# Optimization experiments

Measured on AMD Instinct MI355X. Metric: run time of the kernel, lower is better.

Reference implementation:

```python
import jax, jax.numpy as jnp
import numpy as np
import math

B, T, D, H, L, V = 2, 1024, 768, 12, 4, 50257
HD = D // H
ROPE_PCT = 0.5
MAX_WL = 10000.0
EPS = 1e-5


def setup_inputs() -> dict:
    key = jax.random.key(0)
    ks = jax.random.split(key, 8)
    s = 0.02
    return {
        "idx": jax.random.randint(ks[0], (B, T), 0, V, dtype=jnp.int32),
        "wte": jax.random.normal(ks[1], (V, D), jnp.float32) * s,
        "ln1_g": jnp.ones((L, D), jnp.float32),
        "ln1_b": jnp.zeros((L, D), jnp.float32),
        "Wqkv": jax.random.normal(ks[2], (L, D, 3 * D), jnp.float32) * s,
        "bqkv": jnp.zeros((L, 3 * D), jnp.float32),
        "Wo": jax.random.normal(ks[3], (L, D, D), jnp.float32) * s,
        "bo": jnp.zeros((L, D), jnp.float32),
        "ln2_g": jnp.ones((L, D), jnp.float32),
        "ln2_b": jnp.zeros((L, D), jnp.float32),
        "Wfc": jax.random.normal(ks[4], (L, D, 4 * D), jnp.float32) * s,
        "bfc": jnp.zeros((L, 4 * D), jnp.float32),
        "Wp": jax.random.normal(ks[5], (L, 4 * D, D), jnp.float32) * s,
        "bp": jnp.zeros((L, D), jnp.float32),
        "lnf_g": jnp.ones((D,), jnp.float32),
        "lnf_b": jnp.zeros((D,), jnp.float32),
        "Wlm": jax.random.normal(ks[6], (D, V), jnp.float32) * s,
    }


def _ln(x, g, b):
    m = x.mean(-1, keepdims=True)
    v = x.var(-1, keepdims=True)
    return (x - m) / jnp.sqrt(v + EPS) * g + b


def _gelu(x):
    return 0.5 * x * (1.0 + jnp.tanh(math.sqrt(2.0 / math.pi) * (x + 0.044715 * x ** 3)))


def _p_rope(x, positions):
    # x: [B, H, T, HD]; partial RoPE: rotate first ROPE_PCT of angle pairs, leave rest.
    rope_angles = int(ROPE_PCT * HD // 2)
    nope_angles = HD // 2 - rope_angles
    fraction = 2.0 * jnp.arange(0, rope_angles) / HD
    timescale = jnp.power(MAX_WL, fraction)
    timescale = jnp.pad(timescale, (0, nope_angles), constant_values=jnp.inf)
    sinusoid = positions[:, None] / timescale[None, :]  # [T, HD//2]; pos/inf = 0 -> no rotation
    sin, cos = jnp.sin(sinusoid), jnp.cos(sinusoid)
    first, second = jnp.split(x, 2, axis=-1)
    out = jnp.concatenate([first * cos - second * sin, second * cos + first * sin], axis=-1)
    return out.astype(x.dtype)


def reference(idx, wte, ln1_g, ln1_b, Wqkv, bqkv, Wo, bo, ln2_g, ln2_b, Wfc, bfc, Wp, bp, lnf_g, lnf_b, Wlm):
    x = wte[idx]  # [B, T, D]
    positions = jnp.arange(T, dtype=x.dtype)
    causal = jnp.tril(jnp.ones((T, T), dtype=bool))
    scale = jnp.sqrt(jnp.float32(HD)).astype(x.dtype)
    for l in range(L):
        h1 = _ln(x, ln1_g[l], ln1_b[l])
        h2 = _ln(x, ln2_g[l], ln2_b[l])  # note: both LNs read the same x (as in source)
        # attention
        qkv = h1 @ Wqkv[l] + bqkv[l]
        q, k, v = jnp.split(qkv, 3, axis=-1)
        sh = lambda t: t.reshape(B, T, H, HD).transpose(0, 2, 1, 3)
        q, k, v = sh(q), sh(k), sh(v)
        q = _p_rope(q, positions)
        k = _p_rope(k, positions)
        att = jnp.einsum('bhqd,bhkd->bhqk', q, k) / scale
        att = jnp.where(causal, att, jnp.finfo(att.dtype).min)
        att = jax.nn.softmax(att, axis=-1)
        y = jnp.einsum('bhqk,bhkd->bhqd', att, v)
        y = y.transpose(0, 2, 1, 3).reshape(B, T, D)
        x = x + (y @ Wo[l] + bo[l])
        # MLP
        h = _gelu(h2 @ Wfc[l] + bfc[l])
        x = x + (h @ Wp[l] + bp[l])
    x = _ln(x, lnf_g, lnf_b)
    logits = x @ Wlm  # [B, T, V]
    return logits
```

## Files before the change

### kernel.cpp

```cpp
#include <hip/hip_runtime.h>

typedef unsigned short u16;
typedef unsigned int u32;
typedef __attribute__((ext_vector_type(8))) short bf16x8;
typedef __attribute__((ext_vector_type(4))) float f32x4;

#define SEQ 1024
#define DM 768
#define NH 12
#define HD2 64
#define NLAYER 4
#define NVOCAB 50257
#define BT 2048

__device__ __forceinline__ u16 f2bf(float f) {
  union { float f; u32 u; } v; v.f = f;
  u32 r = v.u + 0x7FFFu + ((v.u >> 16) & 1u);
  return (u16)(r >> 16);
}
__device__ __forceinline__ float bf2f(u16 u) {
  union { u32 u; float f; } v; v.u = ((u32)u) << 16;
  return v.f;
}

__device__ __forceinline__ void glds16(const u16* g, u16* l) {
  __builtin_amdgcn_global_load_lds(
      (const __attribute__((address_space(1))) u32*)(const void*)g,
      (__attribute__((address_space(3))) u32*)(void*)l, 16, 0, 0);
}

__global__ void k_embed(const int* __restrict__ idx, const float* __restrict__ wte,
                        float* __restrict__ xf) {
  int r = blockIdx.x;
  int tok = idx[r];
  const float* s = wte + (size_t)tok * DM;
  float* d = xf + (size_t)r * DM;
  for (int c = threadIdx.x; c < DM; c += 256) d[c] = s[c];
}

__global__ void k_cvtT(const float* __restrict__ in, u16* __restrict__ out,
                       int R, int C) {
  __shared__ u16 t[32][34];
  int c0 = blockIdx.x * 32, r0 = blockIdx.y * 32;
  int tx = threadIdx.x & 31, ty = threadIdx.x >> 5;
#pragma unroll
  for (int i = 0; i < 4; ++i) {
    int r = r0 + ty + i * 8, c = c0 + tx;
    float v = (c < C) ? in[(size_t)r * C + c] : 0.f;
    t[ty + i * 8][tx] = f2bf(v);
  }
  __syncthreads();
  int cy = threadIdx.x >> 4;
  int rx = (threadIdx.x & 15) * 2;
#pragma unroll
  for (int i = 0; i < 2; ++i) {
    int c = c0 + cy + i * 16;
    if (c < C) {
      u32 wv = (u32)t[rx][cy + i * 16] | ((u32)t[rx + 1][cy + i * 16] << 16);
      *(u32*)&out[(size_t)c * R + r0 + rx] = wv;
    }
  }
}

__device__ __forceinline__ float bsum(float v, float* red) {
#pragma unroll
  for (int o = 32; o > 0; o >>= 1) v += __shfl_down(v, o);
  if ((threadIdx.x & 63) == 0) red[threadIdx.x >> 6] = v;
  __syncthreads();
  if (threadIdx.x == 0) red[4] = red[0] + red[1] + red[2] + red[3];
  __syncthreads();
  return red[4];
}

__global__ void k_ln(const float* __restrict__ x, const float* __restrict__ g1,
                     const float* __restrict__ b1, const float* __restrict__ g2,
                     const float* __restrict__ b2, u16* __restrict__ o1,
                     u16* __restrict__ o2) {
  __shared__ float red[8];
  int r = blockIdx.x;
  int t = threadIdx.x;
  const float* xr = x + (size_t)r * DM;
  float v0 = xr[t], v1 = xr[t + 256], v2 = xr[t + 512];
  float mean = bsum(v0 + v1 + v2, red) * (1.f / DM);
  float d0 = v0 - mean, d1 = v1 - mean, d2 = v2 - mean;
  float var = bsum(d0 * d0 + d1 * d1 + d2 * d2, red) * (1.f / DM);
  float rstd = rsqrtf(var + 1e-5f);
  u16* p1 = o1 + (size_t)r * DM;
  p1[t]       = f2bf(d0 * rstd * g1[t]       + b1[t]);
  p1[t + 256] = f2bf(d1 * rstd * g1[t + 256] + b1[t + 256]);
  p1[t + 512] = f2bf(d2 * rstd * g1[t + 512] + b1[t + 512]);
  if (o2) {
    u16* p2 = o2 + (size_t)r * DM;
    p2[t]       = f2bf(d0 * rstd * g2[t]       + b2[t]);
    p2[t + 256] = f2bf(d1 * rstd * g2[t + 256] + b2[t + 256]);
    p2[t + 512] = f2bf(d2 * rstd * g2[t + 512] + b2[t + 512]);
  }
}

__global__ void k_rope(const u16* __restrict__ qkvb, u16* __restrict__ qr,
                       u16* __restrict__ kr) {
  int gid = blockIdx.x * 256 + threadIdx.x;
  int j = gid & 31;
  int h = (gid >> 5) % NH;
  int t = (gid / (32 * NH)) & (SEQ - 1);
  int b = gid / (32 * NH * SEQ);
  float c = 1.f, s = 0.f;
  if (j < 16) {
    float inv = powf(10000.f, -(float)j * (1.f / 32.f));
    float ang = (float)t * inv;
    c = cosf(ang);
    s = sinf(ang);
  }
  size_t base = (size_t)(b * SEQ + t) * (3 * DM);
  size_t ob = ((size_t)(b * NH + h) * SEQ + t) * HD2 + j;
  {
    float a0 = bf2f(qkvb[base + h * HD2 + j]);
    float a1 = bf2f(qkvb[base + h * HD2 + j + 32]);
    qr[ob] = f2bf(a0 * c - a1 * s);
    qr[ob + 32] = f2bf(a1 * c + a0 * s);
  }
  {
    float a0 = bf2f(qkvb[base + DM + h * HD2 + j]);
    float a1 = bf2f(qkvb[base + DM + h * HD2 + j + 32]);
    kr[ob] = f2bf(a0 * c - a1 * s);
    kr[ob + 32] = f2bf(a1 * c + a0 * s);
  }
}

__global__ void k_vtrans(const u16* __restrict__ qkvb, u16* __restrict__ vT) {
  __shared__ u16 tile[64][65];
  int t0 = blockIdx.x * 64;
  int bh = blockIdx.y;
  int b = bh / NH, h = bh % NH;
  int rr = threadIdx.x >> 2, seg = threadIdx.x & 3;
  const u16* src = qkvb + (size_t)(b * SEQ + t0 + rr) * (3 * DM) + 2 * DM + h * HD2;
#pragma unroll
  for (int i = 0; i < 16; ++i) tile[rr][seg * 16 + i] = src[seg * 16 + i];
  __syncthreads();
  u16* dst = vT + ((size_t)bh * HD2 + rr) * SEQ + t0;
#pragma unroll
  for (int i = 0; i < 16; ++i) dst[seg * 16 + i] = tile[seg * 16 + i][rr];
}

__global__ void k_attn(const u16* __restrict__ qr, const u16* __restrict__ kr,
                       const u16* __restrict__ vT, u16* __restrict__ yb) {
  int ti = (int)gridDim.x - 1 - (int)blockIdx.x;
  int bh = blockIdx.y;
  __shared__ u16 Ps[64 * 72];
  __shared__ u16 Ks[64 * 72];
  __shared__ u16 Vs[64 * 72];
  int tid = threadIdx.x;
  int rr = tid >> 2, cc = tid & 3;
  int w = tid >> 6, l = tid & 63;
  int rl = l & 15, g = l >> 4;
  {
    const u16* gq = qr + ((size_t)bh * SEQ + ti * 64 + rr) * HD2;
    *(uint4*)&Ps[rr * 72 + cc * 8]      = *(const uint4*)(gq + cc * 8);
    *(uint4*)&Ps[rr * 72 + cc * 8 + 32] = *(const uint4*)(gq + cc * 8 + 32);
  }
  __syncthreads();
  bf16x8 aq0 = *(const bf16x8*)&Ps[(w * 16 + rl) * 72 + g * 8];
  bf16x8 aq1 = *(const bf16x8*)&Ps[(w * 16 + rl) * 72 + 32 + g * 8];
  float m[4], lsum[4];
  f32x4 oacc[4] = {};
#pragma unroll
  for (int r2 = 0; r2 < 4; ++r2) { m[r2] = -3.0e38f; lsum[r2] = 0.f; }
  const u16* gk = kr + ((size_t)bh * SEQ + rr) * HD2;
  const u16* gv = vT + ((size_t)bh * HD2 + rr) * SEQ;
  int qloc = w * 16 + g * 4;
  for (int kt = 0; kt <= ti; ++kt) {
    __syncthreads();
    {
      const u16* gkk = gk + (size_t)kt * 64 * HD2;
      *(uint4*)&Ks[rr * 72 + cc * 8]      = *(const uint4*)(gkk + cc * 8);
      *(uint4*)&Ks[rr * 72 + cc * 8 + 32] = *(const uint4*)(gkk + cc * 8 + 32);
      *(uint4*)&Vs[rr * 72 + cc * 8]      = *(const uint4*)(gv + kt * 64 + cc * 8);
      *(uint4*)&Vs[rr * 72 + cc * 8 + 32] = *(const uint4*)(gv + kt * 64 + cc * 8 + 32);
    }
    __syncthreads();
    f32x4 s[4] = {};
#pragma unroll
    for (int nt = 0; nt < 4; ++nt) {
      bf16x8 b0 = *(const bf16x8*)&Ks[(nt * 16 + rl) * 72 + g * 8];
      bf16x8 b1 = *(const bf16x8*)&Ks[(nt * 16 + rl) * 72 + 32 + g * 8];
      s[nt] = __builtin_amdgcn_mfma_f32_16x16x32_bf16(aq0, b0, s[nt], 0, 0, 0);
      s[nt] = __builtin_amdgcn_mfma_f32_16x16x32_bf16(aq1, b1, s[nt], 0, 0, 0);
    }
#pragma unroll
    for (int nt = 0; nt < 4; ++nt) s[nt] *= 0.125f;
    if (kt == ti) {
#pragma unroll
      for (int nt = 0; nt < 4; ++nt) {
        int col = nt * 16 + rl;
#pragma unroll
        for (int r2 = 0; r2 < 4; ++r2)
          if (col > qloc + r2) s[nt][r2] = -3.0e38f;
      }
    }
#pragma unroll
    for (int r2 = 0; r2 < 4; ++r2) {
      float pm = fmaxf(fmaxf(s[0][r2], s[1][r2]), fmaxf(s[2][r2], s[3][r2]));
#pragma unroll
      for (int o = 1; o < 16; o <<= 1) pm = fmaxf(pm, __shfl_xor(pm, o));
      float mn = fmaxf(m[r2], pm);
      float corr = __expf(m[r2] - mn);
      float p0 = __expf(s[0][r2] - mn);
      float p1 = __expf(s[1][r2] - mn);
      float p2 = __expf(s[2][r2] - mn);
      float p3 = __expf(s[3][r2] - mn);
      float ps = p0 + p1 + p2 + p3;
#pragma unroll
      for (int o = 1; o < 16; o <<= 1) ps += __shfl_xor(ps, o);
      lsum[r2] = lsum[r2] * corr + ps;
      m[r2] = mn;
      oacc[0][r2] *= corr; oacc[1][r2] *= corr;
      oacc[2][r2] *= corr; oacc[3][r2] *= corr;
      int prow = (qloc + r2) * 72;
      Ps[prow + rl]      = f2bf(p0);
      Ps[prow + 16 + rl] = f2bf(p1);
      Ps[prow + 32 + rl] = f2bf(p2);
      Ps[prow + 48 + rl] = f2bf(p3);
    }
    __syncthreads();
    bf16x8 pa0 = *(const bf16x8*)&Ps[(w * 16 + rl) * 72 + g * 8];
    bf16x8 pa1 = *(const bf16x8*)&Ps[(w * 16 + rl) * 72 + 32 + g * 8];
#pragma unroll
    for (int nt = 0; nt < 4; ++nt) {
      bf16x8 b0 = *(const bf16x8*)&Vs[(nt * 16 + rl) * 72 + g * 8];
      bf16x8 b1 = *(const bf16x8*)&Vs[(nt * 16 + rl) * 72 + 32 + g * 8];
      oacc[nt] = __builtin_amdgcn_mfma_f32_16x16x32_bf16(pa0, b0, oacc[nt], 0, 0, 0);
      oacc[nt] = __builtin_amdgcn_mfma_f32_16x16x32_bf16(pa1, b1, oacc[nt], 0, 0, 0);
    }
  }
  int b = bh / NH, h = bh % NH;
  float invl[4];
#pragma unroll
  for (int r2 = 0; r2 < 4; ++r2) invl[r2] = 1.f / lsum[r2];
#pragma unroll
  for (int nt = 0; nt < 4; ++nt) {
    int d = nt * 16 + rl;
#pragma unroll
    for (int r2 = 0; r2 < 4; ++r2) {
      int trow = ti * 64 + qloc + r2;
      yb[((size_t)(b * SEQ + trow)) * DM + h * HD2 + d] = f2bf(oacc[nt][r2] * invl[r2]);
    }
  }
}

__global__ void k_logits(const u16* __restrict__ A, const u16* __restrict__ Bt,
                         float* __restrict__ outf, int M, int N, int K, int MT) {
  __shared__ u16 SM[16384];
  u16* As = SM;
  u16* Bs = SM + 8192;
  float* cw = (float*)SM;
  int nwg = gridDim.x;
  int id = blockIdx.x;
  if ((nwg & 7) == 0) id = (id & 7) * (nwg >> 3) + (id >> 3);
  int mt = id % MT, nt = id / MT;
  int m0 = mt * 128, n0 = nt * 128;
  int tid = threadIdx.x;
  int w = tid >> 6, l = tid & 63;
  int rbase = w * 8 + (l >> 3);
  int gs = (l & 7) ^ (l >> 3);
  const u16* gA[4];
  const u16* gB[4];
#pragma unroll
  for (int c = 0; c < 4; ++c) {
    gA[c] = A + (size_t)(m0 + c * 32 + rbase) * K + gs * 8;
    int rb = n0 + c * 32 + rbase; if (rb > N - 1) rb = N - 1;
    gB[c] = Bt + (size_t)rb * K + gs * 8;
  }
  u16* dA = As + w * 512;
  u16* dB = Bs + w * 512;
  int wm = (w >> 1) * 64, wn = (w & 1) * 64;
  int rl = l & 15, g = l >> 4;
  int sw = rl & 7;
  f32x4 acc[4][4] = {};
  int nK = K >> 6;
  for (int kt = 0; kt < nK; ++kt) {
    __syncthreads();
#pragma unroll
    for (int c = 0; c < 4; ++c) {
      glds16(gA[c] + kt * 64, dA + c * 2048);
      glds16(gB[c] + kt * 64, dB + c * 2048);
    }
    __syncthreads();
#pragma unroll
    for (int ks = 0; ks < 2; ++ks) {
      bf16x8 af[4], bfr[4];
      int slot = ((ks * 4 + g) ^ sw) * 8;
#pragma unroll
      for (int i = 0; i < 4; ++i)
        af[i] = *(const bf16x8*)&As[(wm + i * 16 + rl) * 64 + slot];
#pragma unroll
      for (int j = 0; j < 4; ++j)
        bfr[j] = *(const bf16x8*)&Bs[(wn + j * 16 + rl) * 64 + slot];
#pragma unroll
      for (int i = 0; i < 4; ++i)
#pragma unroll
        for (int j = 0; j < 4; ++j)
          acc[i][j] = __builtin_amdgcn_mfma_f32_16x16x32_bf16(af[i], bfr[j],
                                                              acc[i][j], 0, 0, 0);
    }
  }
  for (int ch = 0; ch < 4; ++ch) {
    __syncthreads();
    if ((w >> 1) == (ch >> 1)) {
      int ib = (ch & 1) * 2;
#pragma unroll
      for (int ii = 0; ii < 2; ++ii) {
#pragma unroll
        for (int j = 0; j < 4; ++j) {
          int col = wn + j * 16 + rl;
#pragma unroll
          for (int r2 = 0; r2 < 4; ++r2) {
            int rowc = ii * 16 + g * 4 + r2;
            cw[rowc * 132 + col] = acc[ib + ii][j][r2];
          }
        }
      }
    }
    __syncthreads();
    for (int t = tid; t < 4096; t += 256) {
      int rowc = t >> 7, col = t & 127;
      int gc = n0 + col;
      if (gc < N) outf[(size_t)(m0 + ch * 32 + rowc) * N + gc] = cw[rowc * 132 + col];
    }
  }
}

__global__ void k_gemm64(const u16* __restrict__ A, const u16* __restrict__ Bt,
                         const float* __restrict__ bias, u16* __restrict__ outb,
                         float* __restrict__ outf, int M, int N, int K, int MT,
                         int mode) {
  __shared__ u16 As[4096];
  __shared__ u16 Bs[4096];
  int nwg = gridDim.x;
  int id = blockIdx.x;
  if ((nwg & 7) == 0) id = (id & 7) * (nwg >> 3) + (id >> 3);
  int mt = id % MT, nt = id / MT;
  int sk = blockIdx.y, nsk = gridDim.y;
  int Kc = K / nsk, k0 = sk * Kc;
  int m0 = mt * 64, n0 = nt * 64;
  int tid = threadIdx.x;
  int w = tid >> 6, l = tid & 63;
  int row0 = tid >> 3, slot0 = tid & 7;
  int gs0 = slot0 ^ (row0 & 7);
  const u16* gA0 = A + (size_t)(m0 + row0) * K + k0 + gs0 * 8;
  const u16* gA1 = gA0 + (size_t)32 * K;
  const u16* gB0 = Bt + (size_t)(n0 + row0) * K + k0 + gs0 * 8;
  const u16* gB1 = gB0 + (size_t)32 * K;
  u16* dA0 = As + w * 512;
  u16* dA1 = As + 2048 + w * 512;
  u16* dB0 = Bs + w * 512;
  u16* dB1 = Bs + 2048 + w * 512;
  int wm = (w >> 1) * 32, wn = (w & 1) * 32;
  int rl = l & 15, g = l >> 4;
  int sl0 = g ^ (rl & 7), sl1 = (4 + g) ^ (rl & 7);
  f32x4 acc[2][2] = {};
  int nK = Kc >> 6;
  for (int kt = 0; kt < nK; ++kt) {
    __syncthreads();
    glds16(gA0 + kt * 64, dA0);
    glds16(gA1 + kt * 64, dA1);
    glds16(gB0 + kt * 64, dB0);
    glds16(gB1 + kt * 64, dB1);
    __syncthreads();
    bf16x8 a0[2], a1[2], b0[2], b1[2];
#pragma unroll
    for (int i = 0; i < 2; ++i) {
      int r = (wm + i * 16 + rl) * 64;
      a0[i] = *(const bf16x8*)&As[r + sl0 * 8];
      a1[i] = *(const bf16x8*)&As[r + sl1 * 8];
    }
#pragma unroll
    for (int j = 0; j < 2; ++j) {
      int r = (wn + j * 16 + rl) * 64;
      b0[j] = *(const bf16x8*)&Bs[r + sl0 * 8];
      b1[j] = *(const bf16x8*)&Bs[r + sl1 * 8];
    }
#pragma unroll
    for (int i = 0; i < 2; ++i)
#pragma unroll
      for (int j = 0; j < 2; ++j) {
        acc[i][j] = __builtin_amdgcn_mfma_f32_16x16x32_bf16(a0[i], b0[j],
                                                            acc[i][j], 0, 0, 0);
        acc[i][j] = __builtin_amdgcn_mfma_f32_16x16x32_bf16(a1[i], b1[j],
                                                            acc[i][j], 0, 0, 0);
      }
  }
#pragma unroll
  for (int i = 0; i < 2; ++i) {
#pragma unroll
    for (int j = 0; j < 2; ++j) {
      int col = n0 + wn + j * 16 + rl;
      float bv = bias ? bias[col] : 0.f;
#pragma unroll
      for (int r2 = 0; r2 < 4; ++r2) {
        int row = m0 + wm + i * 16 + g * 4 + r2;
        size_t oi = (size_t)row * N + col;
        float v = acc[i][j][r2];
        if (mode == 0) {
          outb[oi] = f2bf(v + bv);
        } else if (mode == 1) {
          v += bv;
          float u = 0.7978845608028654f * (v + 0.044715f * v * v * v);
          outb[oi] = f2bf(0.5f * v * (1.f + tanhf(u)));
        } else {
          if (sk == 0) v += bv;
          atomicAdd(&outf[oi], v);
        }
      }
    }
  }
}

__global__ void k_gemm_f32b(const u16* __restrict__ A, const float* __restrict__ B,
                            float* __restrict__ outf, int M, int N, int K) {
  __shared__ u16 As[128 * 40];
  __shared__ u16 Bs[4 * 128 * 12];
  int tid = threadIdx.x;
  int wid = tid >> 6, lane = tid & 63;
  int rl = lane & 15, g = lane >> 4;
  int m0 = blockIdx.x * 128, n0 = blockIdx.y * 128;
  int wm = (wid >> 1) * 64, wn = (wid & 1) * 64;
  int ar = tid >> 2, ac = tid & 3;
  int bn = tid & 127, bq = tid >> 7;
  f32x4 acc[4][4] = {};
  int nK = K / 32;
  for (int kt = 0; kt < nK; ++kt) {
    __syncthreads();
    {
      const u16* ga = A + (size_t)(m0 + ar) * K + kt * 32 + ac * 8;
      *(uint4*)&As[ar * 40 + ac * 8] = *(const uint4*)ga;
      *(uint4*)&As[(ar + 64) * 40 + ac * 8] = *(const uint4*)(ga + (size_t)64 * K);
    }
    int col = n0 + bn;
#pragma unroll
    for (int r = 0; r < 4; ++r) {
      int kq = bq + 2 * r;
      int kk = kt * 32 + kq * 4;
      float f0 = 0.f, f1 = 0.f, f2v = 0.f, f3 = 0.f;
      if (col < N) {
        const float* gb = B + (size_t)kk * N + col;
        f0 = gb[0]; f1 = gb[(size_t)N]; f2v = gb[(size_t)2 * N]; f3 = gb[(size_t)3 * N];
      }
      uint2 wv;
      wv.x = (u32)f2bf(f0) | ((u32)f2bf(f1) << 16);
      wv.y = (u32)f2bf(f2v) | ((u32)f2bf(f3) << 16);
      *(uint2*)&Bs[(kq >> 1) * 1536 + bn * 12 + (kq & 1) * 4] = wv;
    }
    __syncthreads();
    bf16x8 af[4], bfr[4];
#pragma unroll
    for (int mt = 0; mt < 4; ++mt)
      af[mt] = *(const bf16x8*)&As[(wm + mt * 16 + rl) * 40 + g * 8];
#pragma unroll
    for (int nt = 0; nt < 4; ++nt) {
      const u16* p = &Bs[g * 1536 + (wn + nt * 16 + rl) * 12];
      union { bf16x8 v; uint2 u2[2]; } tmp;
      tmp.u2[0] = *(const uint2*)p;
      tmp.u2[1] = *(const uint2*)(p + 4);
      bfr[nt] = tmp.v;
    }
#pragma unroll
    for (int mt = 0; mt < 4; ++mt)
#pragma unroll
      for (int nt = 0; nt < 4; ++nt)
        acc[mt][nt] = __builtin_amdgcn_mfma_f32_16x16x32_bf16(af[mt], bfr[nt],
                                                              acc[mt][nt], 0, 0, 0);
  }
#pragma unroll
  for (int mt = 0; mt < 4; ++mt)
#pragma unroll
    for (int nt = 0; nt < 4; ++nt) {
      int col = n0 + wn + nt * 16 + rl;
      if (col >= N) continue;
#pragma unroll
      for (int r2 = 0; r2 < 4; ++r2) {
        int row = m0 + wm + mt * 16 + g * 4 + r2;
        outf[(size_t)row * N + col] = acc[mt][nt][r2];
      }
    }
}

extern "C" void kernel_launch(void* const* d_in, const int* in_sizes, int n_in,
                              void* d_out, int out_size, void* d_ws, size_t ws_size,
                              hipStream_t stream) {
  (void)in_sizes; (void)n_in; (void)out_size;
  const int*   idx  = (const int*)  d_in[0];
  const float* wte  = (const float*)d_in[1];
  const float* ln1g = (const float*)d_in[2];
  const float* ln1b = (const float*)d_in[3];
  const float* Wqkv = (const float*)d_in[4];
  const float* bqkv = (const float*)d_in[5];
  const float* Wo   = (const float*)d_in[6];
  const float* bo   = (const float*)d_in[7];
  const float* ln2g = (const float*)d_in[8];
  const float* ln2b = (const float*)d_in[9];
  const float* Wfc  = (const float*)d_in[10];
  const float* bfc  = (const float*)d_in[11];
  const float* Wp   = (const float*)d_in[12];
  const float* bp   = (const float*)d_in[13];
  const float* lnfg = (const float*)d_in[14];
  const float* lnfb = (const float*)d_in[15];
  const float* Wlm  = (const float*)d_in[16];
  float* out = (float*)d_out;

  char* sb = (char*)d_out;
  size_t off = 0;
  auto alloc = [&](size_t bytes) {
    char* p = sb + off;
    off += (bytes + 255) & ~(size_t)255;
    return (void*)p;
  };
  float* xf  = (float*)alloc((size_t)BT * DM * 4);
  u16* h1b   = (u16*)alloc((size_t)BT * DM * 2);
  u16* h2b   = (u16*)alloc((size_t)BT * DM * 2);
  u16* qkvb  = (u16*)alloc((size_t)BT * 3 * DM * 2);
  u16* qr    = (u16*)alloc((size_t)BT * DM * 2);
  u16* kr    = (u16*)alloc((size_t)BT * DM * 2);
  u16* vT    = (u16*)alloc((size_t)BT * DM * 2);
  u16* yb    = (u16*)alloc((size_t)BT * DM * 2);
  u16* hgel  = (u16*)alloc((size_t)BT * 4 * DM * 2);
  u16* wqkvT = (u16*)alloc((size_t)NLAYER * 3 * DM * DM * 2);
  u16* woT   = (u16*)alloc((size_t)NLAYER * DM * DM * 2);
  u16* wfcT  = (u16*)alloc((size_t)NLAYER * 4 * DM * DM * 2);
  u16* wpT   = (u16*)alloc((size_t)NLAYER * 4 * DM * DM * 2);

  size_t wlmT_bytes = (size_t)NVOCAB * DM * 2;
  size_t xlnf_bytes = (size_t)BT * DM * 2;
  bool fast_lm = ws_size >= wlmT_bytes + xlnf_bytes + 512;
  u16* wlmT = (u16*)d_ws;
  u16* xlnf = fast_lm ? (u16*)((char*)d_ws + ((wlmT_bytes + 255) & ~(size_t)255))
                      : (u16*)d_ws;

  for (int l = 0; l < NLAYER; ++l) {
    k_cvtT<<<dim3((3 * DM + 31) / 32, DM / 32), 256, 0, stream>>>(
        Wqkv + (size_t)l * DM * 3 * DM, wqkvT + (size_t)l * 3 * DM * DM, DM, 3 * DM);
    k_cvtT<<<dim3(DM / 32, DM / 32), 256, 0, stream>>>(
        Wo + (size_t)l * DM * DM, woT + (size_t)l * DM * DM, DM, DM);
    k_cvtT<<<dim3((4 * DM) / 32, DM / 32), 256, 0, stream>>>(
        Wfc + (size_t)l * DM * 4 * DM, wfcT + (size_t)l * 4 * DM * DM, DM, 4 * DM);
    k_cvtT<<<dim3(DM / 32, (4 * DM) / 32), 256, 0, stream>>>(
        Wp + (size_t)l * 4 * DM * DM, wpT + (size_t)l * 4 * DM * DM, 4 * DM, DM);
  }
  if (fast_lm)
    k_cvtT<<<dim3((NVOCAB + 31) / 32, DM / 32), 256, 0, stream>>>(Wlm, wlmT, DM, NVOCAB);

  k_embed<<<BT, 256, 0, stream>>>(idx, wte, xf);
  for (int l = 0; l < NLAYER; ++l) {
    k_ln<<<BT, 256, 0, stream>>>(xf, ln1g + l * DM, ln1b + l * DM,
                                 ln2g + l * DM, ln2b + l * DM, h1b, h2b);
    k_gemm64<<<dim3((BT / 64) * (3 * DM / 64), 1), 256, 0, stream>>>(
        h1b, wqkvT + (size_t)l * 3 * DM * DM, bqkv + (size_t)l * 3 * DM,
        qkvb, nullptr, BT, 3 * DM, DM, BT / 64, 0);
    k_rope<<<(2 * SEQ * NH * 32) / 256, 256, 0, stream>>>(qkvb, qr, kr);
    k_vtrans<<<dim3(SEQ / 64, 2 * NH), 256, 0, stream>>>(qkvb, vT);
    k_attn<<<dim3(SEQ / 64, 2 * NH), 256, 0, stream>>>(qr, kr, vT, yb);
    k_gemm64<<<dim3((BT / 64) * (DM / 64), 2), 256, 0, stream>>>(
        yb, woT + (size_t)l * DM * DM, bo + (size_t)l * DM,
        nullptr, xf, BT, DM, DM, BT / 64, 2);
    k_gemm64<<<dim3((BT / 64) * (4 * DM / 64), 1), 256, 0, stream>>>(
        h2b, wfcT + (size_t)l * 4 * DM * DM, bfc + (size_t)l * 4 * DM,
        hgel, nullptr, BT, 4 * DM, DM, BT / 64, 1);
    k_gemm64<<<dim3((BT / 64) * (DM / 64), 4), 256, 0, stream>>>(
        hgel, wpT + (size_t)l * 4 * DM * DM, bp + (size_t)l * DM,
        nullptr, xf, BT, DM, 4 * DM, BT / 64, 2);
  }
  k_ln<<<BT, 256, 0, stream>>>(xf, lnfg, lnfb, nullptr, nullptr, xlnf, nullptr);
  if (fast_lm) {
    int nt = (NVOCAB + 127) / 128;
    k_logits<<<(BT / 128) * nt, 256, 0, stream>>>(
        xlnf, wlmT, out, BT, NVOCAB, DM, BT / 128);
  } else {
    k_gemm_f32b<<<dim3(BT / 128, (NVOCAB + 127) / 128), 256, 0, stream>>>(
        xlnf, Wlm, out, BT, NVOCAB, DM);
  }
}
```

Measured before the change: 1.020 ms.

## Double-buffer LDS tiles with async loads in attention and GEMM kernels

Converts the attention, logits and generic GEMM kernels to a double-buffered LDS scheme. The next K/V or A/B tile is issued with async global-to-LDS loads while MFMAs run on the current tile, which removes one barrier per iteration. The logits kernel also moves to a 32-wide K step with a new swizzle, and all three kernels raise wave priority around the MFMA sections. The logits output is written with nontemporal stores. In exchange this uses more LDS per block, which can lower occupancy, and it depends on the async loads having completed before the single barrier at the end of each iteration.

```diff
diff --git a/kernel.cpp b/kernel.cpp
--- a/kernel.cpp
+++ b/kernel.cpp
@@ -147,8 +147,8 @@
   int ti = (int)gridDim.x - 1 - (int)blockIdx.x;
   int bh = blockIdx.y;
   __shared__ u16 Ps[64 * 72];
-  __shared__ u16 Ks[64 * 72];
-  __shared__ u16 Vs[64 * 72];
+  __shared__ u16 Ks[2][4096];
+  __shared__ u16 Vs[2][4096];
   int tid = threadIdx.x;
   int rr = tid >> 2, cc = tid & 3;
   int w = tid >> 6, l = tid & 63;
@@ -158,6 +158,14 @@
     *(uint4*)&Ps[rr * 72 + cc * 8]      = *(const uint4*)(gq + cc * 8);
     *(uint4*)&Ps[rr * 72 + cc * 8 + 32] = *(const uint4*)(gq + cc * 8 + 32);
   }
+  int srow = w * 8 + (l >> 3);
+  int gs = (l & 7) ^ (l >> 3);
+  const u16* gkb = kr + (size_t)bh * SEQ * HD2;
+  const u16* gvb = vT + (size_t)bh * HD2 * SEQ;
+  glds16(gkb + (size_t)(0 * 64 + srow) * 64 + gs * 8,      &Ks[0][w * 512]);
+  glds16(gkb + (size_t)(0 * 64 + 32 + srow) * 64 + gs * 8, &Ks[0][2048 + w * 512]);
+  glds16(gvb + (size_t)srow * SEQ + 0 * 64 + gs * 8,       &Vs[0][w * 512]);
+  glds16(gvb + (size_t)(32 + srow) * SEQ + 0 * 64 + gs * 8,&Vs[0][2048 + w * 512]);
   __syncthreads();
   bf16x8 aq0 = *(const bf16x8*)&Ps[(w * 16 + rl) * 72 + g * 8];
   bf16x8 aq1 = *(const bf16x8*)&Ps[(w * 16 + rl) * 72 + 32 + g * 8];
@@ -165,27 +173,28 @@
   f32x4 oacc[4] = {};
 #pragma unroll
   for (int r2 = 0; r2 < 4; ++r2) { m[r2] = -3.0e38f; lsum[r2] = 0.f; }
-  const u16* gk = kr + ((size_t)bh * SEQ + rr) * HD2;
-  const u16* gv = vT + ((size_t)bh * HD2 + rr) * SEQ;
   int qloc = w * 16 + g * 4;
+  int sw = rl & 7;
+  int cur = 0;
   for (int kt = 0; kt <= ti; ++kt) {
-    __syncthreads();
-    {
-      const u16* gkk = gk + (size_t)kt * 64 * HD2;
-      *(uint4*)&Ks[rr * 72 + cc * 8]      = *(const uint4*)(gkk + cc * 8);
-      *(uint4*)&Ks[rr * 72 + cc * 8 + 32] = *(const uint4*)(gkk + cc * 8 + 32);
-      *(uint4*)&Vs[rr * 72 + cc * 8]      = *(const uint4*)(gv + kt * 64 + cc * 8);
-      *(uint4*)&Vs[rr * 72 + cc * 8 + 32] = *(const uint4*)(gv + kt * 64 + cc * 8 + 32);
-    }
-    __syncthreads();
+    if (kt < ti) {
+      int nx = cur ^ 1;
+      glds16(gkb + (size_t)((kt + 1) * 64 + srow) * 64 + gs * 8,      &Ks[nx][w * 512]);
+      glds16(gkb + (size_t)((kt + 1) * 64 + 32 + srow) * 64 + gs * 8, &Ks[nx][2048 + w * 512]);
+      glds16(gvb + (size_t)srow * SEQ + (kt + 1) * 64 + gs * 8,       &Vs[nx][w * 512]);
+      glds16(gvb + (size_t)(32 + srow) * SEQ + (kt + 1) * 64 + gs * 8,&Vs[nx][2048 + w * 512]);
+    }
     f32x4 s[4] = {};
+    __builtin_amdgcn_s_setprio(1);
 #pragma unroll
     for (int nt = 0; nt < 4; ++nt) {
-      bf16x8 b0 = *(const bf16x8*)&Ks[(nt * 16 + rl) * 72 + g * 8];
-      bf16x8 b1 = *(const bf16x8*)&Ks[(nt * 16 + rl) * 72 + 32 + g * 8];
+      int r = (nt * 16 + rl) * 64;
+      bf16x8 b0 = *(const bf16x8*)&Ks[cur][r + ((0 + g) ^ sw) * 8];
+      bf16x8 b1 = *(const bf16x8*)&Ks[cur][r + ((4 + g) ^ sw) * 8];
       s[nt] = __builtin_amdgcn_mfma_f32_16x16x32_bf16(aq0, b0, s[nt], 0, 0, 0);
       s[nt] = __builtin_amdgcn_mfma_f32_16x16x32_bf16(aq1, b1, s[nt], 0, 0, 0);
     }
+    __builtin_amdgcn_s_setprio(0);
 #pragma unroll
     for (int nt = 0; nt < 4; ++nt) s[nt] *= 0.125f;
     if (kt == ti) {
@@ -221,16 +230,20 @@
       Ps[prow + 32 + rl] = f2bf(p2);
       Ps[prow + 48 + rl] = f2bf(p3);
     }
-    __syncthreads();
     bf16x8 pa0 = *(const bf16x8*)&Ps[(w * 16 + rl) * 72 + g * 8];
     bf16x8 pa1 = *(const bf16x8*)&Ps[(w * 16 + rl) * 72 + 32 + g * 8];
+    __builtin_amdgcn_s_setprio(1);
 #pragma unroll
     for (int nt = 0; nt < 4; ++nt) {
-      bf16x8 b0 = *(const bf16x8*)&Vs[(nt * 16 + rl) * 72 + g * 8];
-      bf16x8 b1 = *(const bf16x8*)&Vs[(nt * 16 + rl) * 72 + 32 + g * 8];
+      int r = (nt * 16 + rl) * 64;
+      bf16x8 b0 = *(const bf16x8*)&Vs[cur][r + ((0 + g) ^ sw) * 8];
+      bf16x8 b1 = *(const bf16x8*)&Vs[cur][r + ((4 + g) ^ sw) * 8];
       oacc[nt] = __builtin_amdgcn_mfma_f32_16x16x32_bf16(pa0, b0, oacc[nt], 0, 0, 0);
       oacc[nt] = __builtin_amdgcn_mfma_f32_16x16x32_bf16(pa1, b1, oacc[nt], 0, 0, 0);
     }
+    __builtin_amdgcn_s_setprio(0);
+    __syncthreads();
+    cur ^= 1;
   }
   int b = bh / NH, h = bh % NH;
   float invl[4];
@@ -250,8 +263,6 @@
 __global__ void k_logits(const u16* __restrict__ A, const u16* __restrict__ Bt,
                          float* __restrict__ outf, int M, int N, int K, int MT) {
   __shared__ u16 SM[16384];
-  u16* As = SM;
-  u16* Bs = SM + 8192;
   float* cw = (float*)SM;
   int nwg = gridDim.x;
   int id = blockIdx.x;
@@ -260,51 +271,55 @@
   int m0 = mt * 128, n0 = nt * 128;
   int tid = threadIdx.x;
   int w = tid >> 6, l = tid & 63;
-  int rbase = w * 8 + (l >> 3);
-  int gs = (l & 7) ^ (l >> 3);
-  const u16* gA[4];
-  const u16* gB[4];
-#pragma unroll
-  for (int c = 0; c < 4; ++c) {
-    gA[c] = A + (size_t)(m0 + c * 32 + rbase) * K + gs * 8;
-    int rb = n0 + c * 32 + rbase; if (rb > N - 1) rb = N - 1;
-    gB[c] = Bt + (size_t)rb * K + gs * 8;
-  }
-  u16* dA = As + w * 512;
-  u16* dB = Bs + w * 512;
+  int srow = w * 16 + (l >> 2);
+  int gs = (l & 3) ^ ((l >> 3) & 3);
+  const u16* gA0 = A + (size_t)(m0 + srow) * K + gs * 8;
+  const u16* gA1 = A + (size_t)(m0 + 64 + srow) * K + gs * 8;
+  int rb0 = n0 + srow;      if (rb0 > N - 1) rb0 = N - 1;
+  int rb1 = n0 + 64 + srow; if (rb1 > N - 1) rb1 = N - 1;
+  const u16* gB0 = Bt + (size_t)rb0 * K + gs * 8;
+  const u16* gB1 = Bt + (size_t)rb1 * K + gs * 8;
   int wm = (w >> 1) * 64, wn = (w & 1) * 64;
   int rl = l & 15, g = l >> 4;
-  int sw = rl & 7;
+  int sla = g ^ ((rl >> 1) & 3);
   f32x4 acc[4][4] = {};
-  int nK = K >> 6;
+  int nK = K >> 5;
+  int cur = 0;
+  {
+    u16* dA = SM + w * 512;
+    glds16(gA0, dA); glds16(gA1, dA + 2048);
+    u16* dB = SM + 4096 + w * 512;
+    glds16(gB0, dB); glds16(gB1, dB + 2048);
+  }
+  __syncthreads();
   for (int kt = 0; kt < nK; ++kt) {
+    if (kt + 1 < nK) {
+      u16* dA = SM + (cur ^ 1) * 8192 + w * 512;
+      glds16(gA0 + (kt + 1) * 32, dA); glds16(gA1 + (kt + 1) * 32, dA + 2048);
+      u16* dB = dA + 4096;
+      glds16(gB0 + (kt + 1) * 32, dB); glds16(gB1 + (kt + 1) * 32, dB + 2048);
+    }
+    const u16* As = SM + cur * 8192;
+    const u16* Bs = As + 4096;
+    bf16x8 af[4], bfr[4];
+    __builtin_amdgcn_s_setprio(1);
+#pragma unroll
+    for (int i = 0; i < 4; ++i)
+      af[i] = *(const bf16x8*)&As[(wm + i * 16 + rl) * 32 + sla * 8];
+#pragma unroll
+    for (int j = 0; j < 4; ++j)
+      bfr[j] = *(const bf16x8*)&Bs[(wn + j * 16 + rl) * 32 + sla * 8];
+#pragma unroll
+    for (int i = 0; i < 4; ++i)
+#pragma unroll
+      for (int j = 0; j < 4; ++j)
+        acc[i][j] = __builtin_amdgcn_mfma_f32_16x16x32_bf16(af[i], bfr[j],
+                                                            acc[i][j], 0, 0, 0);
+    __builtin_amdgcn_s_setprio(0);
     __syncthreads();
-#pragma unroll
-    for (int c = 0; c < 4; ++c) {
-      glds16(gA[c] + kt * 64, dA + c * 2048);
-      glds16(gB[c] + kt * 64, dB + c * 2048);
-    }
-    __syncthreads();
-#pragma unroll
-    for (int ks = 0; ks < 2; ++ks) {
-      bf16x8 af[4], bfr[4];
-      int slot = ((ks * 4 + g) ^ sw) * 8;
-#pragma unroll
-      for (int i = 0; i < 4; ++i)
-        af[i] = *(const bf16x8*)&As[(wm + i * 16 + rl) * 64 + slot];
-#pragma unroll
-      for (int j = 0; j < 4; ++j)
-        bfr[j] = *(const bf16x8*)&Bs[(wn + j * 16 + rl) * 64 + slot];
-#pragma unroll
-      for (int i = 0; i < 4; ++i)
-#pragma unroll
-        for (int j = 0; j < 4; ++j)
-          acc[i][j] = __builtin_amdgcn_mfma_f32_16x16x32_bf16(af[i], bfr[j],
-                                                              acc[i][j], 0, 0, 0);
-    }
+    cur ^= 1;
   }
   for (int ch = 0; ch < 4; ++ch) {
-    __syncthreads();
     if ((w >> 1) == (ch >> 1)) {
       int ib = (ch & 1) * 2;
 #pragma unroll
@@ -324,8 +339,11 @@
     for (int t = tid; t < 4096; t += 256) {
       int rowc = t >> 7, col = t & 127;
       int gc = n0 + col;
-      if (gc < N) outf[(size_t)(m0 + ch * 32 + rowc) * N + gc] = cw[rowc * 132 + col];
-    }
+      if (gc < N)
+        __builtin_nontemporal_store(cw[rowc * 132 + col],
+                                    &outf[(size_t)(m0 + ch * 32 + rowc) * N + gc]);
+    }
+    __syncthreads();
   }
 }
 
@@ -333,8 +351,8 @@
                          const float* __restrict__ bias, u16* __restrict__ outb,
                          float* __restrict__ outf, int M, int N, int K, int MT,
                          int mode) {
-  __shared__ u16 As[4096];
-  __shared__ u16 Bs[4096];
+  __shared__ u16 As[8192];
+  __shared__ u16 Bs[8192];
   int nwg = gridDim.x;
   int id = blockIdx.x;
   if ((nwg & 7) == 0) id = (id & 7) * (nwg >> 3) + (id >> 3);
@@ -350,34 +368,40 @@
   const u16* gA1 = gA0 + (size_t)32 * K;
   const u16* gB0 = Bt + (size_t)(n0 + row0) * K + k0 + gs0 * 8;
   const u16* gB1 = gB0 + (size_t)32 * K;
-  u16* dA0 = As + w * 512;
-  u16* dA1 = As + 2048 + w * 512;
-  u16* dB0 = Bs + w * 512;
-  u16* dB1 = Bs + 2048 + w * 512;
   int wm = (w >> 1) * 32, wn = (w & 1) * 32;
   int rl = l & 15, g = l >> 4;
   int sl0 = g ^ (rl & 7), sl1 = (4 + g) ^ (rl & 7);
   f32x4 acc[2][2] = {};
   int nK = Kc >> 6;
+  int cur = 0;
+  {
+    glds16(gA0, As + w * 512); glds16(gA1, As + 2048 + w * 512);
+    glds16(gB0, Bs + w * 512); glds16(gB1, Bs + 2048 + w * 512);
+  }
+  __syncthreads();
   for (int kt = 0; kt < nK; ++kt) {
-    __syncthreads();
-    glds16(gA0 + kt * 64, dA0);
-    glds16(gA1 + kt * 64, dA1);
-    glds16(gB0 + kt * 64, dB0);
-    glds16(gB1 + kt * 64, dB1);
-    __syncthreads();
+    if (kt + 1 < nK) {
+      int nx = (cur ^ 1) * 4096;
+      glds16(gA0 + (kt + 1) * 64, As + nx + w * 512);
+      glds16(gA1 + (kt + 1) * 64, As + nx + 2048 + w * 512);
+      glds16(gB0 + (kt + 1) * 64, Bs + nx + w * 512);
+      glds16(gB1 + (kt + 1) * 64, Bs + nx + 2048 + w * 512);
+    }
+    const u16* Ac = As + cur * 4096;
+    const u16* Bc = Bs + cur * 4096;
     bf16x8 a0[2], a1[2], b0[2], b1[2];
+    __builtin_amdgcn_s_setprio(1);
 #pragma unroll
     for (int i = 0; i < 2; ++i) {
       int r = (wm + i * 16 + rl) * 64;
-      a0[i] = *(const bf16x8*)&As[r + sl0 * 8];
-      a1[i] = *(const bf16x8*)&As[r + sl1 * 8];
+      a0[i] = *(const bf16x8*)&Ac[r + sl0 * 8];
+      a1[i] = *(const bf16x8*)&Ac[r + sl1 * 8];
     }
 #pragma unroll
     for (int j = 0; j < 2; ++j) {
       int r = (wn + j * 16 + rl) * 64;
-      b0[j] = *(const bf16x8*)&Bs[r + sl0 * 8];
-      b1[j] = *(const bf16x8*)&Bs[r + sl1 * 8];
+      b0[j] = *(const bf16x8*)&Bc[r + sl0 * 8];
+      b1[j] = *(const bf16x8*)&Bc[r + sl1 * 8];
     }
 #pragma unroll
     for (int i = 0; i < 2; ++i)
@@ -388,6 +412,9 @@
         acc[i][j] = __builtin_amdgcn_mfma_f32_16x16x32_bf16(a1[i], b1[j],
                                                             acc[i][j], 0, 0, 0);
       }
+    __builtin_amdgcn_s_setprio(0);
+    __syncthreads();
+    cur ^= 1;
   }
 #pragma unroll
   for (int i = 0; i < 2; ++i) {
```

Measured after the change: 1.037 ms. Within noise of the previous version (+1.7%).
